# Optimization experiments

Measured on AMD Instinct MI355X. Metric: run time of the kernel, lower is better.

The kernel has to match this reference:

```python
import jax, jax.numpy as jnp
import numpy as np

# Module constants (from init_kwargs)
NB_IN = 4          # num_blocks_in
NB_OUT = 8         # num_blocks_out
BS_IN = 128        # block_size_in (hard-coded in source)
NHID = 4096
BS_OUT = NHID // NB_OUT   # 512, also att_out
TOPK = 4
DK = 64            # d_k = d_v, n_head = 1


def _group_linear(x, w):
    # x: (B, n_blocks, d_in), w: (n_blocks, d_in, d_out) -> (B, n_blocks, d_out)
    return jnp.einsum('bnd,nde->bne', x, w)


def _attend(q, k, v):
    # single-head scaled dot-product attention
    attn = jax.nn.softmax(jnp.einsum('bqd,bkd->bqk', q, k) / jnp.sqrt(jnp.asarray(DK, q.dtype)), axis=-1)
    return jnp.einsum('bqk,bkd->bqd', attn, v), attn


def setup_inputs() -> dict:
    key = jax.random.key(0)
    ks = jax.random.split(key, 20)
    s = 0.02
    d = {
        'inp': jax.random.normal(ks[0], (1024, NB_IN * BS_IN), jnp.float32),
        'hx': jax.random.normal(ks[1], (1024, NHID), jnp.float32),
        'cx': jax.random.normal(ks[2], (1024, NHID), jnp.float32),
        # inp_att (residual=False): GroupLinear q/k/v + fc
        'ia_wq': jax.random.normal(ks[3], (NB_OUT, BS_OUT, DK), jnp.float32) * s,
        'ia_wk': jax.random.normal(ks[4], (NB_IN + 1, BS_IN, DK), jnp.float32) * s,
        'ia_wv': jax.random.normal(ks[5], (NB_IN + 1, BS_IN, DK), jnp.float32) * s,
        'ia_fc_w': jax.random.normal(ks[6], (DK, BS_OUT), jnp.float32) * s,
        'ia_fc_b': jnp.zeros((BS_OUT,), jnp.float32),
        # mha (residual=True, gated)
        'mha_wq': jax.random.normal(ks[7], (NB_OUT, BS_OUT, DK), jnp.float32) * s,
        'mha_wk': jax.random.normal(ks[8], (NB_OUT, BS_OUT, DK), jnp.float32) * s,
        'mha_wv': jax.random.normal(ks[9], (NB_OUT, BS_OUT, DK), jnp.float32) * s,
        'mha_fc_w': jax.random.normal(ks[10], (DK, BS_OUT), jnp.float32) * s,
        'mha_fc_b': jnp.zeros((BS_OUT,), jnp.float32),
        'mha_gate_w': jax.random.normal(ks[11], (DK, BS_OUT), jnp.float32) * s,
        'mha_gate_b': jnp.zeros((BS_OUT,), jnp.float32),
        # block-diagonal LSTM (BlockLSTM after blockify_params): per-block LSTMCell
        'w_ih': jax.random.normal(ks[12], (NB_OUT, BS_OUT, 4 * BS_OUT), jnp.float32) * s,
        'w_hh': jax.random.normal(ks[13], (NB_OUT, BS_OUT, 4 * BS_OUT), jnp.float32) * s,
        'b_ih': jnp.zeros((NB_OUT, 4 * BS_OUT), jnp.float32),
        'b_hh': jnp.zeros((NB_OUT, 4 * BS_OUT), jnp.float32),
    }
    return d


def _forward(inp, hx, cx, ia_wq, ia_wk, ia_wv, ia_fc_w, ia_fc_b,
             mha_wq, mha_wk, mha_wv, mha_fc_w, mha_fc_b, mha_gate_w, mha_gate_b,
             w_ih, w_hh, b_ih, b_hh):
    B = inp.shape[0]
    # --- input attention (inp_att) ---
    x = inp.reshape(B, NB_IN, BS_IN)
    x = jnp.concatenate([x, jnp.zeros_like(x[:, :1])], axis=1)        # append null block -> (B, NB_IN+1, BS_IN)
    hb = hx.reshape(B, NB_OUT, BS_OUT)
    q = _group_linear(hb, ia_wq)                                      # (B, NB_OUT, DK)
    k = _group_linear(x, ia_wk)
    v = _group_linear(x, ia_wv)
    o, iatt = _attend(q, k, v)                                        # o:(B,NB_OUT,DK), iatt:(B,NB_OUT,NB_IN+1)
    inp_use = (o @ ia_fc_w + ia_fc_b).reshape(B, NB_OUT * BS_OUT)     # residual=False path

    # --- top-k block selection mask (detached) ---
    score = iatt[:, :, 0]                                             # (B, NB_OUT)
    thr = jax.lax.top_k(score, TOPK)[0][:, -1]                        # k-th largest per sample
    mask_blk = (score > thr[:, None] - 0.01).astype(hx.dtype)         # (B, NB_OUT)
    mask = jnp.broadcast_to(mask_blk[:, :, None], (B, NB_OUT, BS_OUT)).reshape(B, NHID)
    mask = jax.lax.stop_gradient(mask)

    # --- block-diagonal LSTM update ---
    xb = inp_use.reshape(B, NB_OUT, BS_OUT)
    cb = cx.reshape(B, NB_OUT, BS_OUT)
    gates = (jnp.einsum('bkd,kdg->bkg', xb, w_ih) + b_ih
             + jnp.einsum('bkd,kdg->bkg', hb, w_hh) + b_hh)           # (B, NB_OUT, 4*BS_OUT)
    i_g, f_g, g_g, o_g = jnp.split(gates, 4, axis=-1)
    c_new = jax.nn.sigmoid(f_g) * cb + jax.nn.sigmoid(i_g) * jnp.tanh(g_g)
    h_new = jax.nn.sigmoid(o_g) * jnp.tanh(c_new)                     # (B, NB_OUT, BS_OUT)
    cx_new = c_new.reshape(B, NHID)

    # --- inter-block attention (step_att, residual + gate) ---
    residual = h_new
    q2 = _group_linear(h_new, mha_wq)
    k2 = _group_linear(h_new, mha_wk)
    v2 = _group_linear(h_new, mha_wv)
    o2, _ = _attend(q2, k2, v2)                                       # (B, NB_OUT, DK)
    out = o2 @ mha_fc_w + mha_fc_b
    gate = jax.nn.sigmoid(o2 @ mha_gate_w + mha_gate_b)
    hx_new = (residual + gate * jnp.tanh(out)).reshape(B, NHID)

    # --- masked blend of old / new states ---
    hx_out = mask * hx_new + (1.0 - mask) * hx
    cx_out = mask * cx_new + (1.0 - mask) * cx
    return hx_out, cx_out, mask


def reference(inp, hx, cx, ia_wq, ia_wk, ia_wv, ia_fc_w, ia_fc_b,
              mha_wq, mha_wk, mha_wv, mha_fc_w, mha_fc_b, mha_gate_w, mha_gate_b,
              w_ih, w_hh, b_ih, b_hh):
    return _forward(inp, hx, cx, ia_wq, ia_wk, ia_wv, ia_fc_w, ia_fc_b,
                    mha_wq, mha_wk, mha_wv, mha_fc_w, mha_fc_b, mha_gate_w, mha_gate_b,
                    w_ih, w_hh, b_ih, b_hh)
```

## Files before the change

kernel.cpp:

```cpp
#include <hip/hip_runtime.h>
#include <hip/hip_bf16.h>

#define B_    1024
#define NHID_ 4096
#define NBO   8
#define BSO   512
#define DK_   64

typedef __bf16 bf16;
typedef __bf16 bf16x2 __attribute__((ext_vector_type(2)));
typedef __bf16 bf16x4 __attribute__((ext_vector_type(4)));
typedef __bf16 bf16x8 __attribute__((ext_vector_type(8)));
typedef float  f32x4  __attribute__((ext_vector_type(4)));

__device__ __forceinline__ float sigf(float x){
    float e = __expf(-x);
    return __builtin_amdgcn_rcpf(1.0f + e);
}
__device__ __forceinline__ float ftanh(float x){
    float e = __expf(2.0f*x);
    return 1.0f - 2.0f*__builtin_amdgcn_rcpf(e + 1.0f);
}

__device__ __forceinline__ void gload16(const void* g, void* lds){
    __builtin_amdgcn_global_load_lds((const __attribute__((address_space(1))) unsigned int*)g,
                                     (__attribute__((address_space(3))) unsigned int*)lds,
                                     16, 0, 0);
}

__device__ __forceinline__ void sbar(){
    asm volatile("" ::: "memory");
    __builtin_amdgcn_s_barrier();
    asm volatile("" ::: "memory");
}
#define WAITVM(N) asm volatile("s_waitcnt vmcnt(" #N ")" ::: "memory")

__global__ __launch_bounds__(256) void k_prep(
    const float* __restrict__ w_ih, const float* __restrict__ w_hh,
    const float* __restrict__ hx,
    const float* __restrict__ mha_wq, const float* __restrict__ mha_wk,
    const float* __restrict__ mha_wv, const float* __restrict__ ia_fc_w,
    const float* __restrict__ fc_w, const float* __restrict__ gate_w,
    bf16* __restrict__ wT, bf16* __restrict__ hb16, bf16* __restrict__ wqkvT,
    bf16* __restrict__ iafcT, bf16* __restrict__ fcgT)
{
    int bid = blockIdx.x;
    int t = threadIdx.x;
    if (bid < 4096){
        int c0 = (bid & 31)*64;
        int k0 = ((bid>>5)&7)*64;
        int z  = bid>>8;
        int n = z>>1, which = z&1;
        const float* src = (which ? w_hh : w_ih) + (size_t)n*512*2048;
        __shared__ float tile[64][65];
        #pragma unroll
        for (int it=0; it<4; ++it){
            int idx = t + it*256;
            int r = idx>>4, c4 = (idx&15)*4;
            *(float4*)&tile[r][c4] = *(const float4*)&src[(size_t)(k0+r)*2048 + c0 + c4];
        }
        __syncthreads();
        #pragma unroll
        for (int it=0; it<2; ++it){
            int idx = t + it*256;
            int c = idx>>3, r8 = (idx&7)*8;
            bf16x8 v;
            #pragma unroll
            for (int jj=0;jj<8;++jj) v[jj] = (bf16)tile[r8+jj][c];
            *(bf16x8*)&wT[((size_t)n*2048 + c0 + c)*1024 + which*512 + k0 + r8] = v;
        }
        return;
    }
    int gid = (bid-4096)*256 + t;
    if (gid < 1048576){
        float4 v = ((const float4*)hx)[gid];
        bf16x4 o; o.x=(bf16)v.x; o.y=(bf16)v.y; o.z=(bf16)v.z; o.w=(bf16)v.w;
        *(bf16x4*)&hb16[(size_t)gid*4] = o;
        return;
    }
    int e = gid - 1048576;
    if (e < 786432){
        int col = e >> 9, k = e & 511;
        int n = col / 192, c = col - n*192;
        int p = c >> 6, ee = c & 63;
        const float* s = (p==0) ? mha_wq : ((p==1) ? mha_wk : mha_wv);
        wqkvT[e] = (bf16)s[((size_t)n*512 + k)*64 + ee];
        return;
    }
    e -= 786432;
    if (e < 32768){
        int c = e>>6, k = e&63;
        iafcT[e] = (bf16)ia_fc_w[(size_t)k*512 + c];
        return;
    }
    e -= 32768;
    if (e < 65536){
        int cg = e>>6, k = e&63;
        int ct = cg>>6, j = cg&63;
        const float* s = (j<32) ? fc_w : gate_w;
        int col = ct*32 + (j&31);
        fcgT[e] = (bf16)s[(size_t)k*512 + col];
    }
}

__global__ __launch_bounds__(256) void k_qkv(const float* __restrict__ hx,
                                             const float* __restrict__ inp,
                                             const float* __restrict__ ia_wq,
                                             const float* __restrict__ ia_wk,
                                             const float* __restrict__ ia_wv,
                                             float* __restrict__ qbufH,
                                             float* __restrict__ kbufH,
                                             float* __restrict__ vbufH)
{
    int b0 = blockIdx.x*32, y = blockIdx.y, z = blockIdx.z, t = threadIdx.x;
    int tx = t&15, ty = t>>4;
    __shared__ float Af[32][36];
    __shared__ float W1[32][68];
    __shared__ float W2[32][68];
    if (y < 8){
        int n = y;
        float acc[2][4] = {};
        for (int k0=z*256; k0<z*256+256; k0+=32){
            { int row=t>>3, c4=(t&7)*4;
              *(float4*)&Af[row][c4] = *(const float4*)&hx[(size_t)(b0+row)*4096 + n*512 + k0 + c4]; }
            #pragma unroll
            for (int j=0;j<2;++j){
                int id = j*256 + t;
                int kk = id>>4, e4 = (id&15)*4;
                *(float4*)&W1[kk][e4] = *(const float4*)&ia_wq[(size_t)n*32768 + (size_t)(k0+kk)*64 + e4];
            }
            __syncthreads();
            #pragma unroll
            for (int kk4=0; kk4<8; ++kk4){
                float4 a0 = *(float4*)&Af[ty*2  ][kk4*4];
                float4 a1 = *(float4*)&Af[ty*2+1][kk4*4];
                #pragma unroll
                for (int j=0;j<4;++j){
                    float4 wv = *(float4*)&W1[kk4*4+j][tx*4];
                    float s0 = (j==0)?a0.x:((j==1)?a0.y:((j==2)?a0.z:a0.w));
                    float s1 = (j==0)?a1.x:((j==1)?a1.y:((j==2)?a1.z:a1.w));
                    acc[0][0]+=s0*wv.x; acc[0][1]+=s0*wv.y; acc[0][2]+=s0*wv.z; acc[0][3]+=s0*wv.w;
                    acc[1][0]+=s1*wv.x; acc[1][1]+=s1*wv.y; acc[1][2]+=s1*wv.z; acc[1][3]+=s1*wv.w;
                }
            }
            __syncthreads();
        }
        #pragma unroll
        for (int r=0;r<2;++r){
            float4 o; o.x=acc[r][0]; o.y=acc[r][1]; o.z=acc[r][2]; o.w=acc[r][3];
            *(float4*)&qbufH[((size_t)(z*B_ + b0+ty*2+r))*512 + n*64 + tx*4] = o;
        }
    } else {
        int jb = y-8;
        float ak[2][4] = {}, av[2][4] = {};
        for (int k0=z*64; k0<z*64+64; k0+=32){
            { int row=t>>3, c4=(t&7)*4;
              *(float4*)&Af[row][c4] = *(const float4*)&inp[(size_t)(b0+row)*512 + jb*128 + k0 + c4]; }
            #pragma unroll
            for (int j=0;j<2;++j){
                int id = j*256 + t;
                int kk = id>>4, e4 = (id&15)*4;
                *(float4*)&W1[kk][e4] = *(const float4*)&ia_wk[(size_t)jb*8192 + (size_t)(k0+kk)*64 + e4];
                *(float4*)&W2[kk][e4] = *(const float4*)&ia_wv[(size_t)jb*8192 + (size_t)(k0+kk)*64 + e4];
            }
            __syncthreads();
            #pragma unroll
            for (int kk4=0; kk4<8; ++kk4){
                float4 a0 = *(float4*)&Af[ty*2  ][kk4*4];
                float4 a1 = *(float4*)&Af[ty*2+1][kk4*4];
                #pragma unroll
                for (int j=0;j<4;++j){
                    float4 wk = *(float4*)&W1[kk4*4+j][tx*4];
                    float4 wv = *(float4*)&W2[kk4*4+j][tx*4];
                    float s0 = (j==0)?a0.x:((j==1)?a0.y:((j==2)?a0.z:a0.w));
                    float s1 = (j==0)?a1.x:((j==1)?a1.y:((j==2)?a1.z:a1.w));
                    ak[0][0]+=s0*wk.x; ak[0][1]+=s0*wk.y; ak[0][2]+=s0*wk.z; ak[0][3]+=s0*wk.w;
                    ak[1][0]+=s1*wk.x; ak[1][1]+=s1*wk.y; ak[1][2]+=s1*wk.z; ak[1][3]+=s1*wk.w;
                    av[0][0]+=s0*wv.x; av[0][1]+=s0*wv.y; av[0][2]+=s0*wv.z; av[0][3]+=s0*wv.w;
                    av[1][0]+=s1*wv.x; av[1][1]+=s1*wv.y; av[1][2]+=s1*wv.z; av[1][3]+=s1*wv.w;
                }
            }
            __syncthreads();
        }
        #pragma unroll
        for (int r=0;r<2;++r){
            float4 ok; ok.x=ak[r][0]; ok.y=ak[r][1]; ok.z=ak[r][2]; ok.w=ak[r][3];
            float4 ov; ov.x=av[r][0]; ov.y=av[r][1]; ov.z=av[r][2]; ov.w=av[r][3];
            *(float4*)&kbufH[((size_t)(z*B_ + b0+ty*2+r))*256 + jb*64 + tx*4] = ok;
            *(float4*)&vbufH[((size_t)(z*B_ + b0+ty*2+r))*256 + jb*64 + tx*4] = ov;
        }
    }
}

__global__ __launch_bounds__(256) void k_score(const float* __restrict__ qbufH,
                                               const float* __restrict__ kbufH,
                                               const float* __restrict__ vbufH,
                                               bf16* __restrict__ obuf,
                                               float* __restrict__ maskb,
                                               float* __restrict__ mask_out)
{
    int t = threadIdx.x, sb = t>>6, ts = t&63;
    int b = blockIdx.x*4 + sb;
    __shared__ float q_s[4][512];
    __shared__ float k_s[4][256];
    __shared__ float v_s[4][256];
    __shared__ float at_s[4][40];
    __shared__ float sc_s[4][8];
    __shared__ float mb_s[4][8];

    #pragma unroll
    for (int r=0;r<8;++r){
        int i = ts + r*64;
        q_s[sb][i] = qbufH[(size_t)b*512 + i] + qbufH[(size_t)(B_+b)*512 + i];
    }
    #pragma unroll
    for (int r=0;r<4;++r){
        int i = ts + r*64;
        k_s[sb][i] = kbufH[(size_t)b*256 + i] + kbufH[(size_t)(B_+b)*256 + i];
        v_s[sb][i] = vbufH[(size_t)b*256 + i] + vbufH[(size_t)(B_+b)*256 + i];
    }
    __syncthreads();
    {
        int n = ts>>3, g = ts&7;
        const float* q = &q_s[sb][n*64];
        #pragma unroll
        for (int j=0;j<4;++j){
            const float* k = &k_s[sb][j*64];
            float s = 0.f;
            #pragma unroll
            for (int e=0;e<8;++e) s += q[g*8+e]*k[g*8+e];
            s += __shfl_xor(s, 1);
            s += __shfl_xor(s, 2);
            s += __shfl_xor(s, 4);
            if (g==0) at_s[sb][n*5+j] = s*0.125f;
        }
        if (g==1) at_s[sb][n*5+4] = 0.f;
    }
    __syncthreads();
    if (ts < 8){
        float m = at_s[sb][ts*5];
        for (int j=1;j<5;++j) m = fmaxf(m, at_s[sb][ts*5+j]);
        float ex[5]; float sum=0.f;
        for (int j=0;j<5;++j){ ex[j]=__expf(at_s[sb][ts*5+j]-m); sum+=ex[j]; }
        float inv = 1.f/sum;
        for (int j=0;j<5;++j) at_s[sb][ts*5+j] = ex[j]*inv;
        sc_s[sb][ts] = ex[0]*inv;
    }
    __syncthreads();
    if (ts == 0){
        float s[8];
        for (int nn=0;nn<8;++nn) s[nn] = sc_s[sb][nn];
        for (int ii=1;ii<8;++ii){ float key=s[ii]; int jj=ii-1;
            while(jj>=0 && s[jj]<key){ s[jj+1]=s[jj]; --jj; } s[jj+1]=key; }
        float thr = s[3]-0.01f;
        for (int nn=0;nn<8;++nn) mb_s[sb][nn] = (sc_s[sb][nn] > thr) ? 1.0f : 0.0f;
    }
    __syncthreads();
    #pragma unroll
    for (int r=0;r<8;++r){
        int i = ts + r*64;
        int n = i>>6, e = i&63;
        float s = 0.f;
        #pragma unroll
        for (int j=0;j<4;++j) s += at_s[sb][n*5+j]*v_s[sb][j*64+e];
        obuf[(size_t)b*512 + i] = (bf16)s;
    }
    if (ts < 8) maskb[b*8+ts] = mb_s[sb][ts];
    float4* mo = (float4*)(mask_out + (size_t)b*4096);
    #pragma unroll
    for (int r=0;r<16;++r){
        int i4 = ts + r*64;
        float m = mb_s[sb][i4>>7];
        float4 mv; mv.x=m; mv.y=m; mv.z=m; mv.w=m;
        mo[i4] = mv;
    }
}

__global__ __launch_bounds__(256) void k_fc_ia(const bf16* __restrict__ obuf,
                                               const bf16* __restrict__ iafcT,
                                               const float* __restrict__ ia_fc_b,
                                               bf16* __restrict__ xb16)
{
    int bx = blockIdx.x, by = blockIdx.y;
    int t = threadIdx.x, w = t>>6, l = t&63, quad = l>>4, l16 = l&15;
    int wm = w&1, wd = w>>1;
    __shared__ bf16 A_s[64*72];
    __shared__ bf16 W_s[64*72];
    #pragma unroll
    for (int j=0;j<2;++j){
        int c = t + j*256;
        int row = c>>3, seg = c&7;
        *(bf16x8*)&A_s[row*72 + seg*8] = *(const bf16x8*)&obuf[((size_t)bx*64+row)*64 + seg*8];
        *(bf16x8*)&W_s[row*72 + seg*8] = *(const bf16x8*)&iafcT[((size_t)by*64+row)*64 + seg*8];
    }
    __syncthreads();
    f32x4 zero = {0.f,0.f,0.f,0.f};
    f32x4 acc[2][2] = {{zero,zero},{zero,zero}};
    #pragma unroll
    for (int k0=0;k0<64;k0+=32){
        bf16x8 a[2], bb[2];
        #pragma unroll
        for (int r=0;r<2;++r) a[r] = *(const bf16x8*)&A_s[(wm*32+r*16+l16)*72 + k0 + quad*8];
        #pragma unroll
        for (int c=0;c<2;++c) bb[c] = *(const bf16x8*)&W_s[(wd*32+c*16+l16)*72 + k0 + quad*8];
        #pragma unroll
        for (int r=0;r<2;++r)
            #pragma unroll
            for (int c=0;c<2;++c)
                acc[r][c] = __builtin_amdgcn_mfma_f32_16x16x32_bf16(a[r], bb[c], acc[r][c], 0,0,0);
    }
    #pragma unroll
    for (int c=0;c<2;++c){
        int col = by*64 + wd*32 + c*16 + l16;
        float bias = ia_fc_b[col];
        #pragma unroll
        for (int r=0;r<2;++r)
            #pragma unroll
            for (int v=0;v<4;++v){
                int row = bx*64 + wm*32 + r*16 + quad*4 + v;
                xb16[(size_t)row*512 + col] = (bf16)(acc[r][c][v] + bias);
            }
    }
}

__global__ __launch_bounds__(256,2) void k_lstm(
    const bf16* __restrict__ xb16, const bf16* __restrict__ hb16,
    const bf16* __restrict__ wT, const float* __restrict__ b_ih,
    const float* __restrict__ b_hh, const float* __restrict__ cx,
    const float* __restrict__ maskb,
    float* __restrict__ cx_out, bf16* __restrict__ hn16)
{
    int bid = blockIdx.x;
    int n  = bid & 7;
    int i  = bid >> 3;
    int mt = i & 7, ct = i >> 3;
    int b0 = mt*128, d0 = ct*64;

    int t = threadIdx.x;
    int w = t >> 6, l = t & 63;
    int wm = w & 1, wg = w >> 1;
    int quad = l >> 4, l16 = l & 15;

    __shared__ __align__(16) bf16 lds[3*12288];

    int GA0 = (w*2)*64 + l, GA1 = GA0 + 64;
    int rA0 = GA0>>2,       rA1 = GA1>>2;
    int kA0 = (GA0&3) ^ ((rA0>>1)&3);
    int kA1 = (GA1&3) ^ ((rA1>>1)&3);
    const bf16* xbP0 = xb16 + (size_t)(b0+rA0)*4096 + n*512 + kA0*8;
    const bf16* xbP1 = xb16 + (size_t)(b0+rA1)*4096 + n*512 + kA1*8;
    const bf16* hbP0 = hb16 + (size_t)(b0+rA0)*4096 + n*512 + kA0*8;
    const bf16* hbP1 = hb16 + (size_t)(b0+rA1)*4096 + n*512 + kA1*8;

    const bf16* wbn = wT + (size_t)n*2048*1024;
    int GB0 = (w*4)*64 + l, GB1 = GB0+64, GB2 = GB0+128, GB3 = GB0+192;
    int vc0 = GB0>>2, vc1 = GB1>>2, vc2 = GB2>>2, vc3 = GB3>>2;
    int kB0 = (GB0&3) ^ ((vc0>>1)&3);
    int kB1 = (GB1&3) ^ ((vc1>>1)&3);
    int kB2 = (GB2&3) ^ ((vc2>>1)&3);
    int kB3 = (GB3&3) ^ ((vc3>>1)&3);
    const bf16* wP0 = wbn + (size_t)((vc0>>6)*512 + d0 + (vc0&63))*1024 + kB0*8;
    const bf16* wP1 = wbn + (size_t)((vc1>>6)*512 + d0 + (vc1&63))*1024 + kB1*8;
    const bf16* wP2 = wbn + (size_t)((vc2>>6)*512 + d0 + (vc2&63))*1024 + kB2*8;
    const bf16* wP3 = wbn + (size_t)((vc3>>6)*512 + d0 + (vc3&63))*1024 + kB3*8;

    int offA[4], offB[8];
    #pragma unroll
    for (int m=0;m<4;++m){ int R = wm*64 + m*16 + l16; offA[m] = (R*4 + (quad ^ ((R>>1)&3)))*8; }
    #pragma unroll
    for (int nf=0;nf<8;++nf){ int C = wg*128 + nf*16 + l16; offB[nf] = 4096 + (C*4 + (quad ^ ((C>>1)&3)))*8; }

    auto stA = [&](int buf, int kt){
        const bf16* s0 = (kt<16 ? xbP0 : hbP0) + (kt&15)*32;
        const bf16* s1 = (kt<16 ? xbP1 : hbP1) + (kt&15)*32;
        bf16* dst = &lds[buf*12288 + (w*2)*512];
        gload16(s0, dst);
        gload16(s1, dst + 512);
    };
    auto stB01 = [&](int buf, int kt){
        bf16* dst = &lds[buf*12288 + 4096 + (w*4)*512];
        gload16(wP0 + (size_t)kt*32, dst);
        gload16(wP1 + (size_t)kt*32, dst + 512);
    };
    auto stB23 = [&](int buf, int kt){
        bf16* dst = &lds[buf*12288 + 4096 + (w*4)*512];
        gload16(wP2 + (size_t)kt*32, dst + 1024);
        gload16(wP3 + (size_t)kt*32, dst + 1536);
    };

    f32x4 zero = {0.f,0.f,0.f,0.f};
    f32x4 acc[4][8];
    #pragma unroll
    for (int m=0;m<4;++m)
        #pragma unroll
        for (int nf=0;nf<8;++nf) acc[m][nf] = zero;

    stA(0,0); stB01(0,0); stB23(0,0);
    stA(1,1); stB01(1,1); stB23(1,1);
    WAITVM(6);
    sbar();

    int buf = 0, pbuf = 2;
    #pragma unroll 1
    for (int kt=0; kt<32; ++kt){
        const bf16* base = &lds[buf*12288];
        bf16x8 av[4], bv[4];

        if (kt < 30){ stA(pbuf, kt+2); stB01(pbuf, kt+2); }
        #pragma unroll
        for (int m=0;m<4;++m) av[m] = *(const bf16x8*)&base[offA[m]];
        #pragma unroll
        for (int nf=0;nf<4;++nf) bv[nf] = *(const bf16x8*)&base[offB[nf]];
        __builtin_amdgcn_s_setprio(1);
        #pragma unroll
        for (int m=0;m<4;++m)
            #pragma unroll
            for (int nf=0;nf<4;++nf)
                acc[m][nf] = __builtin_amdgcn_mfma_f32_16x16x32_bf16(av[m], bv[nf], acc[m][nf], 0,0,0);
        __builtin_amdgcn_s_setprio(0);
        sbar();

        if (kt < 30) stB23(pbuf, kt+2);
        #pragma unroll
        for (int nf=0;nf<4;++nf) bv[nf] = *(const bf16x8*)&base[offB[4+nf]];
        __builtin_amdgcn_s_setprio(1);
        #pragma unroll
        for (int m=0;m<4;++m)
            #pragma unroll
            for (int nf=0;nf<4;++nf)
                acc[m][4+nf] = __builtin_amdgcn_mfma_f32_16x16x32_bf16(av[m], bv[nf], acc[m][4+nf], 0,0,0);
        __builtin_amdgcn_s_setprio(0);
        if (kt < 30) { WAITVM(6); } else { WAITVM(0); }
        sbar();
        pbuf = buf; buf = (buf==2) ? 0 : buf+1;
    }

    float* gbuf = (float*)lds;
    const int GP = 260;
    int dl_t = t & 63;
    int i_t  = t >> 6;
    int d = d0 + dl_t;
    float bi  = b_ih[n*2048 +        d] + b_hh[n*2048 +        d];
    float bff = b_ih[n*2048 +  512 + d] + b_hh[n*2048 +  512 + d];
    float bg  = b_ih[n*2048 + 1024 + d] + b_hh[n*2048 + 1024 + d];
    float bo  = b_ih[n*2048 + 1536 + d] + b_hh[n*2048 + 1536 + d];

    #pragma unroll
    for (int c=0; c<2; ++c){
        if (wm == c){
            #pragma unroll
            for (int mm=0; mm<4; ++mm)
                #pragma unroll
                for (int nf=0; nf<8; ++nf)
                    #pragma unroll
                    for (int v=0; v<4; ++v)
                        gbuf[(mm*16 + quad*4 + v)*GP + wg*128 + nf*16 + l16] = acc[mm][nf][v];
        }
        __syncthreads();
        #pragma unroll
        for (int r=0; r<16; ++r){
            int row_l = i_t*16 + r;
            int row_g = b0 + c*64 + row_l;
            float gi = gbuf[row_l*GP +       dl_t] + bi;
            float gf = gbuf[row_l*GP +  64 + dl_t] + bff;
            float gg = gbuf[row_l*GP + 128 + dl_t] + bg;
            float go = gbuf[row_l*GP + 192 + dl_t] + bo;
            size_t gidx = (size_t)row_g*4096 + n*512 + d;
            float cb = cx[gidx];
            float cn = sigf(gf)*cb + sigf(gi)*ftanh(gg);
            float hn = sigf(go)*ftanh(cn);
            float mk = maskb[row_g*8 + n];
            cx_out[gidx] = (mk != 0.f) ? cn : cb;
            hn16[gidx]   = (bf16)hn;
        }
        __syncthreads();
    }
}

__global__ __launch_bounds__(256) void k_proj64(const bf16* __restrict__ hn16,
                                                const bf16* __restrict__ wqkvT,
                                                float* __restrict__ qkv2)
{
    int b0 = blockIdx.x*64, n = blockIdx.y, ct = blockIdx.z;
    int t = threadIdx.x, w = t>>6, l = t&63, quad = l>>4, l16 = l&15;
    int wm = w&1, wd = w>>1;
    __shared__ bf16 A_s[2][256*8];
    __shared__ bf16 B_s[2][256*8];
    f32x4 zero = {0.f,0.f,0.f,0.f};
    f32x4 acc[2][2] = {{zero,zero},{zero,zero}};
    const bf16* ab = hn16 + (size_t)n*512;
    const bf16* wb = wqkvT + ((size_t)n*192 + ct*64)*512;

    auto stage = [&](int buf, int k0){
        int row = t>>2, ss = t&3;
        int seg = ss ^ ((row>>1)&3);
        gload16(ab + (size_t)(b0+row)*4096 + k0 + seg*8, &A_s[buf][(w*64)*8]);
        gload16(wb + (size_t)row*512      + k0 + seg*8, &B_s[buf][(w*64)*8]);
    };

    stage(0, 0);
    for (int it=0; it<16; ++it){
        __syncthreads();
        if (it < 15) stage((it+1)&1, (it+1)*32);
        int buf = it&1;
        bf16x8 a[2], bb[2];
        #pragma unroll
        for (int r=0;r<2;++r){
            int row = wm*32 + r*16 + l16;
            int slot = row*4 + (quad ^ ((row>>1)&3));
            a[r] = *(const bf16x8*)&A_s[buf][slot*8];
        }
        #pragma unroll
        for (int c=0;c<2;++c){
            int col = wd*32 + c*16 + l16;
            int slot = col*4 + (quad ^ ((col>>1)&3));
            bb[c] = *(const bf16x8*)&B_s[buf][slot*8];
        }
        #pragma unroll
        for (int r=0;r<2;++r)
            #pragma unroll
            for (int c=0;c<2;++c)
                acc[r][c] = __builtin_amdgcn_mfma_f32_16x16x32_bf16(a[r], bb[c], acc[r][c], 0,0,0);
    }
    #pragma unroll
    for (int c=0;c<2;++c){
        int col = ct*64 + wd*32 + c*16 + l16;
        #pragma unroll
        for (int r=0;r<2;++r)
            #pragma unroll
            for (int v=0;v<4;++v){
                int row = b0 + wm*32 + r*16 + quad*4 + v;
                qkv2[(size_t)row*1536 + n*192 + col] = acc[r][c][v];
            }
    }
}

__global__ __launch_bounds__(256) void k_att2(const float* __restrict__ qkv2,
                                              bf16* __restrict__ o2buf)
{
    int t = threadIdx.x, sb = t>>6, ts = t&63;
    int b = blockIdx.x*4 + sb;
    __shared__ float q_s[4][512];
    __shared__ float k_s[4][512];
    __shared__ float v_s[4][512];
    __shared__ float at_s[4][64];
    #pragma unroll
    for (int r=0;r<8;++r){
        int i = ts + r*64;
        int n = i>>6, e = i&63;
        const float* src = qkv2 + (size_t)b*1536 + n*192;
        q_s[sb][i] = src[e];
        k_s[sb][i] = src[64+e];
        v_s[sb][i] = src[128+e];
    }
    __syncthreads();
    {
        int n = ts>>3, g = ts&7;
        const float* q = &q_s[sb][n*64];
        #pragma unroll
        for (int j=0;j<8;++j){
            const float* k = &k_s[sb][j*64];
            float s = 0.f;
            #pragma unroll
            for (int e=0;e<8;++e) s += q[g*8+e]*k[g*8+e];
            s += __shfl_xor(s, 1);
            s += __shfl_xor(s, 2);
            s += __shfl_xor(s, 4);
            if (g==0) at_s[sb][n*8+j] = s*0.125f;
        }
    }
    __syncthreads();
    if (ts < 8){
        float m = at_s[sb][ts*8];
        for (int j=1;j<8;++j) m = fmaxf(m, at_s[sb][ts*8+j]);
        float ex[8]; float sum=0.f;
        for (int j=0;j<8;++j){ ex[j]=__expf(at_s[sb][ts*8+j]-m); sum+=ex[j]; }
        float inv = 1.f/sum;
        for (int j=0;j<8;++j) at_s[sb][ts*8+j] = ex[j]*inv;
    }
    __syncthreads();
    #pragma unroll
    for (int r=0;r<8;++r){
        int i = ts + r*64;
        int n = i>>6, e = i&63;
        float s = 0.f;
        #pragma unroll
        for (int j=0;j<8;++j) s += at_s[sb][n*8+j]*v_s[sb][j*64+e];
        o2buf[(size_t)b*512 + i] = (bf16)s;
    }
}

__global__ __launch_bounds__(256) void k_fcgate(const bf16* __restrict__ o2buf,
                                                const bf16* __restrict__ fcgT,
                                                const float* __restrict__ fc_b,
                                                const float* __restrict__ gate_b,
                                                const bf16* __restrict__ hn16,
                                                const float* __restrict__ hx,
                                                const float* __restrict__ maskb,
                                                float* __restrict__ hx_out)
{
    int bx = blockIdx.x, ct0 = blockIdx.y*2;
    int t = threadIdx.x, w = t>>6, l = t&63, quad = l>>4, l16 = l&15;
    __shared__ bf16 A_s[64*72];
    __shared__ bf16 W_s[2][64*72];
    #pragma unroll
    for (int j=0;j<2;++j){
        int c = t + j*256;
        int row = c>>3, seg = c&7;
        *(bf16x8*)&A_s[row*72 + seg*8] = *(const bf16x8*)&o2buf[((size_t)bx*64+row)*64 + seg*8];
        *(bf16x8*)&W_s[0][row*72 + seg*8] = *(const bf16x8*)&fcgT[((size_t)ct0*64+row)*64 + seg*8];
        *(bf16x8*)&W_s[1][row*72 + seg*8] = *(const bf16x8*)&fcgT[((size_t)(ct0+1)*64+row)*64 + seg*8];
    }
    __syncthreads();
    f32x4 zero = {0.f,0.f,0.f,0.f};
    #pragma unroll
    for (int cc=0; cc<2; ++cc){
        int ct = ct0 + cc;
        f32x4 acc[4] = {zero,zero,zero,zero};
        #pragma unroll
        for (int k0=0;k0<64;k0+=32){
            bf16x8 a = *(const bf16x8*)&A_s[(w*16+l16)*72 + k0 + quad*8];
            #pragma unroll
            for (int c=0;c<4;++c){
                bf16x8 bb = *(const bf16x8*)&W_s[cc][(c*16+l16)*72 + k0 + quad*8];
                acc[c] = __builtin_amdgcn_mfma_f32_16x16x32_bf16(a, bb, acc[c], 0,0,0);
            }
        }
        #pragma unroll
        for (int c=0;c<2;++c){
            int d = ct*32 + c*16 + l16;
            float fb = fc_b[d], gb = gate_b[d];
            #pragma unroll
            for (int v=0;v<4;++v){
                int row = bx*64 + w*16 + quad*4 + v;
                int b = row>>3, n = row&7;
                size_t idx = (size_t)b*4096 + n*512 + d;
                float f = acc[c][v]   + fb;
                float g = acc[c+2][v] + gb;
                float hn = (float)hn16[idx];
                float m = maskb[row];
                hx_out[idx] = (m != 0.f) ? (hn + sigf(g)*ftanh(f)) : hx[idx];
            }
        }
    }
}

extern "C" void kernel_launch(void* const* d_in, const int* in_sizes, int n_in,
                              void* d_out, int out_size, void* d_ws, size_t ws_size,
                              hipStream_t stream)
{
    const float* inp       = (const float*)d_in[0];
    const float* hx        = (const float*)d_in[1];
    const float* cx        = (const float*)d_in[2];
    const float* ia_wq     = (const float*)d_in[3];
    const float* ia_wk     = (const float*)d_in[4];
    const float* ia_wv     = (const float*)d_in[5];
    const float* ia_fc_w   = (const float*)d_in[6];
    const float* ia_fc_b   = (const float*)d_in[7];
    const float* mha_wq    = (const float*)d_in[8];
    const float* mha_wk    = (const float*)d_in[9];
    const float* mha_wv    = (const float*)d_in[10];
    const float* mha_fc_w  = (const float*)d_in[11];
    const float* mha_fc_b  = (const float*)d_in[12];
    const float* mha_gate_w= (const float*)d_in[13];
    const float* mha_gate_b= (const float*)d_in[14];
    const float* w_ih      = (const float*)d_in[15];
    const float* w_hh      = (const float*)d_in[16];
    const float* b_ih      = (const float*)d_in[17];
    const float* b_hh      = (const float*)d_in[18];

    float* hx_out  = (float*)d_out;
    float* cx_out  = hx_out + (size_t)B_*NHID_;
    float* mask_out= cx_out + (size_t)B_*NHID_;

    char* p = (char*)d_ws;
    bf16* wT     = (bf16*)p;               p += (size_t)8*2048*1024*2;
    bf16* hb16   = (bf16*)p;               p += (size_t)B_*NHID_*2;
    bf16* xb16   = (bf16*)p;               p += (size_t)B_*NHID_*2;
    bf16* hn16   = (bf16*)p;               p += (size_t)B_*NHID_*2;
    bf16* wqkvT  = (bf16*)p;               p += (size_t)8*192*512*2;
    bf16* iafcT  = (bf16*)p;               p += (size_t)512*64*2;
    bf16* fcgT   = (bf16*)p;               p += (size_t)1024*64*2;
    float* qbufH = (float*)p;              p += (size_t)2*B_*512*4;
    float* kbufH = (float*)p;              p += (size_t)2*B_*256*4;
    float* vbufH = (float*)p;              p += (size_t)2*B_*256*4;
    bf16* obuf   = (bf16*)p;               p += (size_t)B_*8*64*2;
    bf16* o2buf  = (bf16*)p;               p += (size_t)B_*8*64*2;
    float* qkv2  = (float*)p;              p += (size_t)B_*1536*4;
    float* maskb = (float*)p;              p += (size_t)B_*8*4;

    hipLaunchKernelGGL(k_prep, dim3(11648), dim3(256), 0, stream,
                       w_ih, w_hh, hx, mha_wq, mha_wk, mha_wv, ia_fc_w, mha_fc_w, mha_gate_w,
                       wT, hb16, wqkvT, iafcT, fcgT);
    hipLaunchKernelGGL(k_qkv, dim3(32,12,2), dim3(256), 0, stream,
                       hx, inp, ia_wq, ia_wk, ia_wv, qbufH, kbufH, vbufH);
    hipLaunchKernelGGL(k_score, dim3(256), dim3(256), 0, stream,
                       qbufH, kbufH, vbufH, obuf, maskb, mask_out);
    hipLaunchKernelGGL(k_fc_ia, dim3(128,8), dim3(256), 0, stream, obuf, iafcT, ia_fc_b, xb16);
    hipLaunchKernelGGL(k_lstm, dim3(512), dim3(256), 0, stream,
                       xb16, hb16, wT, b_ih, b_hh, cx, maskb, cx_out, hn16);
    hipLaunchKernelGGL(k_proj64, dim3(16,8,3), dim3(256), 0, stream, hn16, wqkvT, qkv2);
    hipLaunchKernelGGL(k_att2, dim3(256), dim3(256), 0, stream, qkv2, o2buf);
    hipLaunchKernelGGL(k_fcgate, dim3(128,8), dim3(256), 0, stream,
                       o2buf, fcgT, mha_fc_b, mha_gate_b, hn16, hx, maskb, hx_out);
}
```

Measured before the change: 283.4 us.

## Fuse qkv into prep, fc into score, and fc-gate into att2 kernels

Merges the input-attention qkv projection into the weight-prep kernel as extra blocks, fuses the input-attention output projection into the score kernel via MFMA on an LDS-staged o tile, and fuses the mha fc/gate projection with the inter-block attention kernel. This removes three launches and the obuf/o2buf round trips through global memory. In exchange, the fused att2fc kernel holds 32 f32x4 accumulators per thread and reads weights straight from global memory without LDS staging, so register pressure rises and only 256 blocks carry the fc work.

```diff
diff --git a/kernel.cpp b/kernel.cpp
--- a/kernel.cpp
+++ b/kernel.cpp
@@ -35,24 +35,112 @@
 }
 #define WAITVM(N) asm volatile("s_waitcnt vmcnt(" #N ")" ::: "memory")
 
-__global__ __launch_bounds__(256) void k_prep(
+__global__ __launch_bounds__(256) void k_prepqkv(
     const float* __restrict__ w_ih, const float* __restrict__ w_hh,
-    const float* __restrict__ hx,
+    const float* __restrict__ hx, const float* __restrict__ inp,
+    const float* __restrict__ ia_wq, const float* __restrict__ ia_wk,
+    const float* __restrict__ ia_wv,
     const float* __restrict__ mha_wq, const float* __restrict__ mha_wk,
     const float* __restrict__ mha_wv, const float* __restrict__ ia_fc_w,
     const float* __restrict__ fc_w, const float* __restrict__ gate_w,
     bf16* __restrict__ wT, bf16* __restrict__ hb16, bf16* __restrict__ wqkvT,
-    bf16* __restrict__ iafcT, bf16* __restrict__ fcgT)
+    bf16* __restrict__ iafcT, bf16* __restrict__ fcgT,
+    float* __restrict__ qbufH, float* __restrict__ kbufH, float* __restrict__ vbufH)
 {
     int bid = blockIdx.x;
     int t = threadIdx.x;
+    __shared__ float Af[32][36];
+    __shared__ float W1[32][68];
+    __shared__ float W2[32][68];
+    __shared__ float tile[64][65];
+
+    if (bid < 768){
+        int z = (bid >= 384) ? 1 : 0;
+        int r = bid - z*384;
+        int y = r >> 5, b0 = (r & 31)*32;
+        int tx = t&15, ty = t>>4;
+        if (y < 8){
+            int n = y;
+            float acc[2][4] = {};
+            for (int k0=z*256; k0<z*256+256; k0+=32){
+                { int row=t>>3, c4=(t&7)*4;
+                  *(float4*)&Af[row][c4] = *(const float4*)&hx[(size_t)(b0+row)*4096 + n*512 + k0 + c4]; }
+                #pragma unroll
+                for (int j=0;j<2;++j){
+                    int id = j*256 + t;
+                    int kk = id>>4, e4 = (id&15)*4;
+                    *(float4*)&W1[kk][e4] = *(const float4*)&ia_wq[(size_t)n*32768 + (size_t)(k0+kk)*64 + e4];
+                }
+                __syncthreads();
+                #pragma unroll
+                for (int kk4=0; kk4<8; ++kk4){
+                    float4 a0 = *(float4*)&Af[ty*2  ][kk4*4];
+                    float4 a1 = *(float4*)&Af[ty*2+1][kk4*4];
+                    #pragma unroll
+                    for (int j=0;j<4;++j){
+                        float4 wv = *(float4*)&W1[kk4*4+j][tx*4];
+                        float s0 = (j==0)?a0.x:((j==1)?a0.y:((j==2)?a0.z:a0.w));
+                        float s1 = (j==0)?a1.x:((j==1)?a1.y:((j==2)?a1.z:a1.w));
+                        acc[0][0]+=s0*wv.x; acc[0][1]+=s0*wv.y; acc[0][2]+=s0*wv.z; acc[0][3]+=s0*wv.w;
+                        acc[1][0]+=s1*wv.x; acc[1][1]+=s1*wv.y; acc[1][2]+=s1*wv.z; acc[1][3]+=s1*wv.w;
+                    }
+                }
+                __syncthreads();
+            }
+            #pragma unroll
+            for (int r2=0;r2<2;++r2){
+                float4 o; o.x=acc[r2][0]; o.y=acc[r2][1]; o.z=acc[r2][2]; o.w=acc[r2][3];
+                *(float4*)&qbufH[((size_t)(z*B_ + b0+ty*2+r2))*512 + n*64 + tx*4] = o;
+            }
+        } else {
+            int jb = y-8;
+            float ak[2][4] = {}, av[2][4] = {};
+            for (int k0=z*64; k0<z*64+64; k0+=32){
+                { int row=t>>3, c4=(t&7)*4;
+                  *(float4*)&Af[row][c4] = *(const float4*)&inp[(size_t)(b0+row)*512 + jb*128 + k0 + c4]; }
+                #pragma unroll
+                for (int j=0;j<2;++j){
+                    int id = j*256 + t;
+                    int kk = id>>4, e4 = (id&15)*4;
+                    *(float4*)&W1[kk][e4] = *(const float4*)&ia_wk[(size_t)jb*8192 + (size_t)(k0+kk)*64 + e4];
+                    *(float4*)&W2[kk][e4] = *(const float4*)&ia_wv[(size_t)jb*8192 + (size_t)(k0+kk)*64 + e4];
+                }
+                __syncthreads();
+                #pragma unroll
+                for (int kk4=0; kk4<8; ++kk4){
+                    float4 a0 = *(float4*)&Af[ty*2  ][kk4*4];
+                    float4 a1 = *(float4*)&Af[ty*2+1][kk4*4];
+                    #pragma unroll
+                    for (int j=0;j<4;++j){
+                        float4 wk = *(float4*)&W1[kk4*4+j][tx*4];
+                        float4 wv = *(float4*)&W2[kk4*4+j][tx*4];
+                        float s0 = (j==0)?a0.x:((j==1)?a0.y:((j==2)?a0.z:a0.w));
+                        float s1 = (j==0)?a1.x:((j==1)?a1.y:((j==2)?a1.z:a1.w));
+                        ak[0][0]+=s0*wk.x; ak[0][1]+=s0*wk.y; ak[0][2]+=s0*wk.z; ak[0][3]+=s0*wk.w;
+                        ak[1][0]+=s1*wk.x; ak[1][1]+=s1*wk.y; ak[1][2]+=s1*wk.z; ak[1][3]+=s1*wk.w;
+                        av[0][0]+=s0*wv.x; av[0][1]+=s0*wv.y; av[0][2]+=s0*wv.z; av[0][3]+=s0*wv.w;
+                        av[1][0]+=s1*wv.x; av[1][1]+=s1*wv.y; av[1][2]+=s1*wv.z; av[1][3]+=s1*wv.w;
+                    }
+                }
+                __syncthreads();
+            }
+            #pragma unroll
+            for (int r2=0;r2<2;++r2){
+                float4 ok; ok.x=ak[r2][0]; ok.y=ak[r2][1]; ok.z=ak[r2][2]; ok.w=ak[r2][3];
+                float4 ov; ov.x=av[r2][0]; ov.y=av[r2][1]; ov.z=av[r2][2]; ov.w=av[r2][3];
+                *(float4*)&kbufH[((size_t)(z*B_ + b0+ty*2+r2))*256 + jb*64 + tx*4] = ok;
+                *(float4*)&vbufH[((size_t)(z*B_ + b0+ty*2+r2))*256 + jb*64 + tx*4] = ov;
+            }
+        }
+        return;
+    }
+    bid -= 768;
     if (bid < 4096){
         int c0 = (bid & 31)*64;
         int k0 = ((bid>>5)&7)*64;
         int z  = bid>>8;
         int n = z>>1, which = z&1;
         const float* src = (which ? w_hh : w_ih) + (size_t)n*512*2048;
-        __shared__ float tile[64][65];
         #pragma unroll
         for (int it=0; it<4; ++it){
             int idx = t + it*256;
@@ -103,99 +191,12 @@
     }
 }
 
-__global__ __launch_bounds__(256) void k_qkv(const float* __restrict__ hx,
-                                             const float* __restrict__ inp,
-                                             const float* __restrict__ ia_wq,
-                                             const float* __restrict__ ia_wk,
-                                             const float* __restrict__ ia_wv,
-                                             float* __restrict__ qbufH,
-                                             float* __restrict__ kbufH,
-                                             float* __restrict__ vbufH)
-{
-    int b0 = blockIdx.x*32, y = blockIdx.y, z = blockIdx.z, t = threadIdx.x;
-    int tx = t&15, ty = t>>4;
-    __shared__ float Af[32][36];
-    __shared__ float W1[32][68];
-    __shared__ float W2[32][68];
-    if (y < 8){
-        int n = y;
-        float acc[2][4] = {};
-        for (int k0=z*256; k0<z*256+256; k0+=32){
-            { int row=t>>3, c4=(t&7)*4;
-              *(float4*)&Af[row][c4] = *(const float4*)&hx[(size_t)(b0+row)*4096 + n*512 + k0 + c4]; }
-            #pragma unroll
-            for (int j=0;j<2;++j){
-                int id = j*256 + t;
-                int kk = id>>4, e4 = (id&15)*4;
-                *(float4*)&W1[kk][e4] = *(const float4*)&ia_wq[(size_t)n*32768 + (size_t)(k0+kk)*64 + e4];
-            }
-            __syncthreads();
-            #pragma unroll
-            for (int kk4=0; kk4<8; ++kk4){
-                float4 a0 = *(float4*)&Af[ty*2  ][kk4*4];
-                float4 a1 = *(float4*)&Af[ty*2+1][kk4*4];
-                #pragma unroll
-                for (int j=0;j<4;++j){
-                    float4 wv = *(float4*)&W1[kk4*4+j][tx*4];
-                    float s0 = (j==0)?a0.x:((j==1)?a0.y:((j==2)?a0.z:a0.w));
-                    float s1 = (j==0)?a1.x:((j==1)?a1.y:((j==2)?a1.z:a1.w));
-                    acc[0][0]+=s0*wv.x; acc[0][1]+=s0*wv.y; acc[0][2]+=s0*wv.z; acc[0][3]+=s0*wv.w;
-                    acc[1][0]+=s1*wv.x; acc[1][1]+=s1*wv.y; acc[1][2]+=s1*wv.z; acc[1][3]+=s1*wv.w;
-                }
-            }
-            __syncthreads();
-        }
-        #pragma unroll
-        for (int r=0;r<2;++r){
-            float4 o; o.x=acc[r][0]; o.y=acc[r][1]; o.z=acc[r][2]; o.w=acc[r][3];
-            *(float4*)&qbufH[((size_t)(z*B_ + b0+ty*2+r))*512 + n*64 + tx*4] = o;
-        }
-    } else {
-        int jb = y-8;
-        float ak[2][4] = {}, av[2][4] = {};
-        for (int k0=z*64; k0<z*64+64; k0+=32){
-            { int row=t>>3, c4=(t&7)*4;
-              *(float4*)&Af[row][c4] = *(const float4*)&inp[(size_t)(b0+row)*512 + jb*128 + k0 + c4]; }
-            #pragma unroll
-            for (int j=0;j<2;++j){
-                int id = j*256 + t;
-                int kk = id>>4, e4 = (id&15)*4;
-                *(float4*)&W1[kk][e4] = *(const float4*)&ia_wk[(size_t)jb*8192 + (size_t)(k0+kk)*64 + e4];
-                *(float4*)&W2[kk][e4] = *(const float4*)&ia_wv[(size_t)jb*8192 + (size_t)(k0+kk)*64 + e4];
-            }
-            __syncthreads();
-            #pragma unroll
-            for (int kk4=0; kk4<8; ++kk4){
-                float4 a0 = *(float4*)&Af[ty*2  ][kk4*4];
-                float4 a1 = *(float4*)&Af[ty*2+1][kk4*4];
-                #pragma unroll
-                for (int j=0;j<4;++j){
-                    float4 wk = *(float4*)&W1[kk4*4+j][tx*4];
-                    float4 wv = *(float4*)&W2[kk4*4+j][tx*4];
-                    float s0 = (j==0)?a0.x:((j==1)?a0.y:((j==2)?a0.z:a0.w));
-                    float s1 = (j==0)?a1.x:((j==1)?a1.y:((j==2)?a1.z:a1.w));
-                    ak[0][0]+=s0*wk.x; ak[0][1]+=s0*wk.y; ak[0][2]+=s0*wk.z; ak[0][3]+=s0*wk.w;
-                    ak[1][0]+=s1*wk.x; ak[1][1]+=s1*wk.y; ak[1][2]+=s1*wk.z; ak[1][3]+=s1*wk.w;
-                    av[0][0]+=s0*wv.x; av[0][1]+=s0*wv.y; av[0][2]+=s0*wv.z; av[0][3]+=s0*wv.w;
-                    av[1][0]+=s1*wv.x; av[1][1]+=s1*wv.y; av[1][2]+=s1*wv.z; av[1][3]+=s1*wv.w;
-                }
-            }
-            __syncthreads();
-        }
-        #pragma unroll
-        for (int r=0;r<2;++r){
-            float4 ok; ok.x=ak[r][0]; ok.y=ak[r][1]; ok.z=ak[r][2]; ok.w=ak[r][3];
-            float4 ov; ov.x=av[r][0]; ov.y=av[r][1]; ov.z=av[r][2]; ov.w=av[r][3];
-            *(float4*)&kbufH[((size_t)(z*B_ + b0+ty*2+r))*256 + jb*64 + tx*4] = ok;
-            *(float4*)&vbufH[((size_t)(z*B_ + b0+ty*2+r))*256 + jb*64 + tx*4] = ov;
-        }
-    }
-}
-
 __global__ __launch_bounds__(256) void k_score(const float* __restrict__ qbufH,
                                                const float* __restrict__ kbufH,
                                                const float* __restrict__ vbufH,
-                                               bf16* __restrict__ obuf,
+                                               const bf16* __restrict__ iafcT,
+                                               const float* __restrict__ ia_fc_b,
+                                               bf16* __restrict__ xb16,
                                                float* __restrict__ maskb,
                                                float* __restrict__ mask_out)
 {
@@ -207,6 +208,7 @@
     __shared__ float at_s[4][40];
     __shared__ float sc_s[4][8];
     __shared__ float mb_s[4][8];
+    __shared__ bf16 o_s[32][72];
 
     #pragma unroll
     for (int r=0;r<8;++r){
@@ -258,12 +260,10 @@
     __syncthreads();
     #pragma unroll
     for (int r=0;r<8;++r){
-        int i = ts + r*64;
-        int n = i>>6, e = i&63;
         float s = 0.f;
         #pragma unroll
-        for (int j=0;j<4;++j) s += at_s[sb][n*5+j]*v_s[sb][j*64+e];
-        obuf[(size_t)b*512 + i] = (bf16)s;
+        for (int j=0;j<4;++j) s += at_s[sb][r*5+j]*v_s[sb][j*64+ts];
+        o_s[sb*8+r][ts] = (bf16)s;
     }
     if (ts < 8) maskb[b*8+ts] = mb_s[sb][ts];
     float4* mo = (float4*)(mask_out + (size_t)b*4096);
@@ -274,52 +274,28 @@
         float4 mv; mv.x=m; mv.y=m; mv.z=m; mv.w=m;
         mo[i4] = mv;
     }
-}
-
-__global__ __launch_bounds__(256) void k_fc_ia(const bf16* __restrict__ obuf,
-                                               const bf16* __restrict__ iafcT,
-                                               const float* __restrict__ ia_fc_b,
-                                               bf16* __restrict__ xb16)
-{
-    int bx = blockIdx.x, by = blockIdx.y;
-    int t = threadIdx.x, w = t>>6, l = t&63, quad = l>>4, l16 = l&15;
-    int wm = w&1, wd = w>>1;
-    __shared__ bf16 A_s[64*72];
-    __shared__ bf16 W_s[64*72];
-    #pragma unroll
-    for (int j=0;j<2;++j){
-        int c = t + j*256;
-        int row = c>>3, seg = c&7;
-        *(bf16x8*)&A_s[row*72 + seg*8] = *(const bf16x8*)&obuf[((size_t)bx*64+row)*64 + seg*8];
-        *(bf16x8*)&W_s[row*72 + seg*8] = *(const bf16x8*)&iafcT[((size_t)by*64+row)*64 + seg*8];
-    }
-    __syncthreads();
-    f32x4 zero = {0.f,0.f,0.f,0.f};
-    f32x4 acc[2][2] = {{zero,zero},{zero,zero}};
-    #pragma unroll
-    for (int k0=0;k0<64;k0+=32){
-        bf16x8 a[2], bb[2];
-        #pragma unroll
-        for (int r=0;r<2;++r) a[r] = *(const bf16x8*)&A_s[(wm*32+r*16+l16)*72 + k0 + quad*8];
-        #pragma unroll
-        for (int c=0;c<2;++c) bb[c] = *(const bf16x8*)&W_s[(wd*32+c*16+l16)*72 + k0 + quad*8];
-        #pragma unroll
-        for (int r=0;r<2;++r)
-            #pragma unroll
-            for (int c=0;c<2;++c)
-                acc[r][c] = __builtin_amdgcn_mfma_f32_16x16x32_bf16(a[r], bb[c], acc[r][c], 0,0,0);
-    }
-    #pragma unroll
-    for (int c=0;c<2;++c){
-        int col = by*64 + wd*32 + c*16 + l16;
-        float bias = ia_fc_b[col];
-        #pragma unroll
-        for (int r=0;r<2;++r)
-            #pragma unroll
-            for (int v=0;v<4;++v){
-                int row = bx*64 + wm*32 + r*16 + quad*4 + v;
-                xb16[(size_t)row*512 + col] = (bf16)(acc[r][c][v] + bias);
+    __syncthreads();
+    {
+        int w = t>>6, l = t&63, quad = l>>4, l16 = l&15;
+        int wm = w&1, wd = w>>1;
+        bf16x8 a0 = *(const bf16x8*)&o_s[wm*16 + l16][quad*8];
+        bf16x8 a1 = *(const bf16x8*)&o_s[wm*16 + l16][32 + quad*8];
+        f32x4 zero = {0.f,0.f,0.f,0.f};
+        #pragma unroll
+        for (int nt=0; nt<16; ++nt){
+            int cg = wd*256 + nt*16 + l16;
+            bf16x8 b0 = *(const bf16x8*)&iafcT[(size_t)cg*64 + quad*8];
+            bf16x8 b1 = *(const bf16x8*)&iafcT[(size_t)cg*64 + 32 + quad*8];
+            f32x4 acc = __builtin_amdgcn_mfma_f32_16x16x32_bf16(a0, b0, zero, 0,0,0);
+            acc = __builtin_amdgcn_mfma_f32_16x16x32_bf16(a1, b1, acc, 0,0,0);
+            float bias = ia_fc_b[cg];
+            #pragma unroll
+            for (int v=0; v<4; ++v){
+                int rm = wm*16 + quad*4 + v;
+                int bb = blockIdx.x*4 + (rm>>3), nn = rm&7;
+                xb16[(size_t)bb*4096 + nn*512 + cg] = (bf16)(acc[v] + bias);
             }
+        }
     }
 }
 
@@ -535,62 +511,7 @@
     }
 }
 
-__global__ __launch_bounds__(256) void k_att2(const float* __restrict__ qkv2,
-                                              bf16* __restrict__ o2buf)
-{
-    int t = threadIdx.x, sb = t>>6, ts = t&63;
-    int b = blockIdx.x*4 + sb;
-    __shared__ float q_s[4][512];
-    __shared__ float k_s[4][512];
-    __shared__ float v_s[4][512];
-    __shared__ float at_s[4][64];
-    #pragma unroll
-    for (int r=0;r<8;++r){
-        int i = ts + r*64;
-        int n = i>>6, e = i&63;
-        const float* src = qkv2 + (size_t)b*1536 + n*192;
-        q_s[sb][i] = src[e];
-        k_s[sb][i] = src[64+e];
-        v_s[sb][i] = src[128+e];
-    }
-    __syncthreads();
-    {
-        int n = ts>>3, g = ts&7;
-        const float* q = &q_s[sb][n*64];
-        #pragma unroll
-        for (int j=0;j<8;++j){
-            const float* k = &k_s[sb][j*64];
-            float s = 0.f;
-            #pragma unroll
-            for (int e=0;e<8;++e) s += q[g*8+e]*k[g*8+e];
-            s += __shfl_xor(s, 1);
-            s += __shfl_xor(s, 2);
-            s += __shfl_xor(s, 4);
-            if (g==0) at_s[sb][n*8+j] = s*0.125f;
-        }
-    }
-    __syncthreads();
-    if (ts < 8){
-        float m = at_s[sb][ts*8];
-        for (int j=1;j<8;++j) m = fmaxf(m, at_s[sb][ts*8+j]);
-        float ex[8]; float sum=0.f;
-        for (int j=0;j<8;++j){ ex[j]=__expf(at_s[sb][ts*8+j]-m); sum+=ex[j]; }
-        float inv = 1.f/sum;
-        for (int j=0;j<8;++j) at_s[sb][ts*8+j] = ex[j]*inv;
-    }
-    __syncthreads();
-    #pragma unroll
-    for (int r=0;r<8;++r){
-        int i = ts + r*64;
-        int n = i>>6, e = i&63;
-        float s = 0.f;
-        #pragma unroll
-        for (int j=0;j<8;++j) s += at_s[sb][n*8+j]*v_s[sb][j*64+e];
-        o2buf[(size_t)b*512 + i] = (bf16)s;
-    }
-}
-
-__global__ __launch_bounds__(256) void k_fcgate(const bf16* __restrict__ o2buf,
+__global__ __launch_bounds__(256) void k_att2fc(const float* __restrict__ qkv2,
                                                 const bf16* __restrict__ fcgT,
                                                 const float* __restrict__ fc_b,
                                                 const float* __restrict__ gate_b,
@@ -599,47 +520,89 @@
                                                 const float* __restrict__ maskb,
                                                 float* __restrict__ hx_out)
 {
-    int bx = blockIdx.x, ct0 = blockIdx.y*2;
-    int t = threadIdx.x, w = t>>6, l = t&63, quad = l>>4, l16 = l&15;
-    __shared__ bf16 A_s[64*72];
-    __shared__ bf16 W_s[2][64*72];
-    #pragma unroll
-    for (int j=0;j<2;++j){
-        int c = t + j*256;
-        int row = c>>3, seg = c&7;
-        *(bf16x8*)&A_s[row*72 + seg*8] = *(const bf16x8*)&o2buf[((size_t)bx*64+row)*64 + seg*8];
-        *(bf16x8*)&W_s[0][row*72 + seg*8] = *(const bf16x8*)&fcgT[((size_t)ct0*64+row)*64 + seg*8];
-        *(bf16x8*)&W_s[1][row*72 + seg*8] = *(const bf16x8*)&fcgT[((size_t)(ct0+1)*64+row)*64 + seg*8];
-    }
-    __syncthreads();
-    f32x4 zero = {0.f,0.f,0.f,0.f};
-    #pragma unroll
-    for (int cc=0; cc<2; ++cc){
-        int ct = ct0 + cc;
-        f32x4 acc[4] = {zero,zero,zero,zero};
-        #pragma unroll
-        for (int k0=0;k0<64;k0+=32){
-            bf16x8 a = *(const bf16x8*)&A_s[(w*16+l16)*72 + k0 + quad*8];
-            #pragma unroll
-            for (int c=0;c<4;++c){
-                bf16x8 bb = *(const bf16x8*)&W_s[cc][(c*16+l16)*72 + k0 + quad*8];
-                acc[c] = __builtin_amdgcn_mfma_f32_16x16x32_bf16(a, bb, acc[c], 0,0,0);
-            }
-        }
-        #pragma unroll
-        for (int c=0;c<2;++c){
-            int d = ct*32 + c*16 + l16;
-            float fb = fc_b[d], gb = gate_b[d];
-            #pragma unroll
-            for (int v=0;v<4;++v){
-                int row = bx*64 + w*16 + quad*4 + v;
-                int b = row>>3, n = row&7;
-                size_t idx = (size_t)b*4096 + n*512 + d;
-                float f = acc[c][v]   + fb;
-                float g = acc[c+2][v] + gb;
-                float hn = (float)hn16[idx];
-                float m = maskb[row];
-                hx_out[idx] = (m != 0.f) ? (hn + sigf(g)*ftanh(f)) : hx[idx];
+    int t = threadIdx.x, sb = t>>6, ts = t&63;
+    int b = blockIdx.x*4 + sb;
+    __shared__ float q_s[4][512];
+    __shared__ float k_s[4][512];
+    __shared__ float v_s[4][512];
+    __shared__ float at_s[4][64];
+    __shared__ bf16 o_s[32][72];
+    #pragma unroll
+    for (int r=0;r<8;++r){
+        int i = ts + r*64;
+        int n = i>>6, e = i&63;
+        const float* src = qkv2 + (size_t)b*1536 + n*192;
+        q_s[sb][i] = src[e];
+        k_s[sb][i] = src[64+e];
+        v_s[sb][i] = src[128+e];
+    }
+    __syncthreads();
+    {
+        int n = ts>>3, g = ts&7;
+        const float* q = &q_s[sb][n*64];
+        #pragma unroll
+        for (int j=0;j<8;++j){
+            const float* k = &k_s[sb][j*64];
+            float s = 0.f;
+            #pragma unroll
+            for (int e=0;e<8;++e) s += q[g*8+e]*k[g*8+e];
+            s += __shfl_xor(s, 1);
+            s += __shfl_xor(s, 2);
+            s += __shfl_xor(s, 4);
+            if (g==0) at_s[sb][n*8+j] = s*0.125f;
+        }
+    }
+    __syncthreads();
+    if (ts < 8){
+        float m = at_s[sb][ts*8];
+        for (int j=1;j<8;++j) m = fmaxf(m, at_s[sb][ts*8+j]);
+        float ex[8]; float sum=0.f;
+        for (int j=0;j<8;++j){ ex[j]=__expf(at_s[sb][ts*8+j]-m); sum+=ex[j]; }
+        float inv = 1.f/sum;
+        for (int j=0;j<8;++j) at_s[sb][ts*8+j] = ex[j]*inv;
+    }
+    __syncthreads();
+    #pragma unroll
+    for (int r=0;r<8;++r){
+        float s = 0.f;
+        #pragma unroll
+        for (int j=0;j<8;++j) s += at_s[sb][r*8+j]*v_s[sb][j*64+ts];
+        o_s[sb*8+r][ts] = (bf16)s;
+    }
+    __syncthreads();
+    {
+        int w = t>>6, l = t&63, quad = l>>4, l16 = l&15;
+        int wm = w&1, wd = w>>1;
+        bf16x8 a0 = *(const bf16x8*)&o_s[wm*16 + l16][quad*8];
+        bf16x8 a1 = *(const bf16x8*)&o_s[wm*16 + l16][32 + quad*8];
+        f32x4 zero = {0.f,0.f,0.f,0.f};
+        f32x4 acc[32];
+        #pragma unroll
+        for (int nt=0; nt<32; ++nt){
+            int cg = wd*512 + nt*16 + l16;
+            bf16x8 b0 = *(const bf16x8*)&fcgT[(size_t)cg*64 + quad*8];
+            bf16x8 b1 = *(const bf16x8*)&fcgT[(size_t)cg*64 + 32 + quad*8];
+            acc[nt] = __builtin_amdgcn_mfma_f32_16x16x32_bf16(a0, b0, zero, 0,0,0);
+            acc[nt] = __builtin_amdgcn_mfma_f32_16x16x32_bf16(a1, b1, acc[nt], 0,0,0);
+        }
+        #pragma unroll
+        for (int ctl=0; ctl<8; ++ctl){
+            #pragma unroll
+            for (int s=0; s<2; ++s){
+                int d = (wd*8+ctl)*32 + s*16 + l16;
+                float fb = fc_b[d], gb = gate_b[d];
+                f32x4 fa = acc[ctl*4+s], ga = acc[ctl*4+2+s];
+                #pragma unroll
+                for (int v=0; v<4; ++v){
+                    int rm = wm*16 + quad*4 + v;
+                    int bb = blockIdx.x*4 + (rm>>3), nn = rm&7;
+                    size_t idx = (size_t)bb*4096 + nn*512 + d;
+                    float f = fa[v] + fb;
+                    float g = ga[v] + gb;
+                    float hnv = (float)hn16[idx];
+                    float mk = maskb[bb*8+nn];
+                    hx_out[idx] = (mk != 0.f) ? (hnv + sigf(g)*ftanh(f)) : hx[idx];
+                }
             }
         }
     }
@@ -684,23 +647,18 @@
     float* qbufH = (float*)p;              p += (size_t)2*B_*512*4;
     float* kbufH = (float*)p;              p += (size_t)2*B_*256*4;
     float* vbufH = (float*)p;              p += (size_t)2*B_*256*4;
-    bf16* obuf   = (bf16*)p;               p += (size_t)B_*8*64*2;
-    bf16* o2buf  = (bf16*)p;               p += (size_t)B_*8*64*2;
     float* qkv2  = (float*)p;              p += (size_t)B_*1536*4;
     float* maskb = (float*)p;              p += (size_t)B_*8*4;
 
-    hipLaunchKernelGGL(k_prep, dim3(11648), dim3(256), 0, stream,
-                       w_ih, w_hh, hx, mha_wq, mha_wk, mha_wv, ia_fc_w, mha_fc_w, mha_gate_w,
-                       wT, hb16, wqkvT, iafcT, fcgT);
-    hipLaunchKernelGGL(k_qkv, dim3(32,12,2), dim3(256), 0, stream,
-                       hx, inp, ia_wq, ia_wk, ia_wv, qbufH, kbufH, vbufH);
+    hipLaunchKernelGGL(k_prepqkv, dim3(12416), dim3(256), 0, stream,
+                       w_ih, w_hh, hx, inp, ia_wq, ia_wk, ia_wv,
+                       mha_wq, mha_wk, mha_wv, ia_fc_w, mha_fc_w, mha_gate_w,
+                       wT, hb16, wqkvT, iafcT, fcgT, qbufH, kbufH, vbufH);
     hipLaunchKernelGGL(k_score, dim3(256), dim3(256), 0, stream,
-                       qbufH, kbufH, vbufH, obuf, maskb, mask_out);
-    hipLaunchKernelGGL(k_fc_ia, dim3(128,8), dim3(256), 0, stream, obuf, iafcT, ia_fc_b, xb16);
+                       qbufH, kbufH, vbufH, iafcT, ia_fc_b, xb16, maskb, mask_out);
     hipLaunchKernelGGL(k_lstm, dim3(512), dim3(256), 0, stream,
                        xb16, hb16, wT, b_ih, b_hh, cx, maskb, cx_out, hn16);
     hipLaunchKernelGGL(k_proj64, dim3(16,8,3), dim3(256), 0, stream, hn16, wqkvT, qkv2);
-    hipLaunchKernelGGL(k_att2, dim3(256), dim3(256), 0, stream, qkv2, o2buf);
-    hipLaunchKernelGGL(k_fcgate, dim3(128,8), dim3(256), 0, stream,
-                       o2buf, fcgT, mha_fc_b, mha_gate_b, hn16, hx, maskb, hx_out);
-}
+    hipLaunchKernelGGL(k_att2fc, dim3(256), dim3(256), 0, stream,
+                       qkv2, fcgT, mha_fc_b, mha_gate_b, hn16, hx, maskb, hx_out);
+}
```

Result: no change. 284.3 us (+0.3%).
